# Performance work log

Measured on AMD Instinct MI355X. Metric: run time of the kernel, lower is better.

## Reference

```python
import jax, jax.numpy as jnp
import numpy as np

HEAD_DIM = 32
KSIZE = 3
SCALE = HEAD_DIM ** (-0.5)  # self.scale = head_dim ** -0.5 with head_dim=32


def setup_inputs() -> dict:
    key = jax.random.key(0)
    kq, kk, kv = jax.random.split(key, 3)
    shape = (4, 128, 128, 128)  # (B, d, H, W)
    return {
        "q": jax.random.normal(kq, shape, dtype=jnp.float32),
        "k": jax.random.normal(kk, shape, dtype=jnp.float32),
        "v": jax.random.normal(kv, shape, dtype=jnp.float32),
    }


def _unfold3(x):
    # nn.Unfold(kernel_size=3, dilation=1, padding=1, stride=1):
    # [B, d, H, W] -> [B, d, 9, H, W], kernel positions in row-major (ki, kj)
    B, d, H, W = x.shape
    xp = jnp.pad(x, ((0, 0), (0, 0), (1, 1), (1, 1)))
    return jnp.stack(
        [xp[:, :, i:i + H, j:j + W] for i in range(KSIZE) for j in range(KSIZE)],
        axis=2,
    )


def reference(q, k, v):
    B, d, H, W = q.shape
    h = d // HEAD_DIM  # number of heads
    n = H * W
    # q: [B, h, head_dim, n]
    qh = q.reshape(B, h, HEAD_DIM, n)
    # k patches: [B, h, head_dim, 9, n]
    kp = _unfold3(k).reshape(B, h, HEAD_DIM, KSIZE * KSIZE, n)
    # attn: [B, h, n, 9] = (q . k_neighbor) * scale, softmax over the 9 neighbors
    attn = jnp.einsum('bhcn,bhckn->bhnk', qh, kp) * SCALE
    attn = jax.nn.softmax(attn, axis=-1)
    # v patches: [B, h, head_dim, 9, n]
    vp = _unfold3(v).reshape(B, h, HEAD_DIM, KSIZE * KSIZE, n)
    # out: [B, n, h, head_dim] -> [B, H, W, d] (head-major channel layout, as in torch)
    out = jnp.einsum('bhnk,bhckn->bnhc', attn, vp).reshape(B, H, W, d)
    return jax.nn.relu(out)
```

## Files before the change

kernel.cpp:

```cpp
#include <hip/hip_runtime.h>

#define HW 128
#define PLANE (HW * HW)
#define SCALE 0.17677669529663687f

__global__ __launch_bounds__(256, 2) void natt3x3_kernel(
    const float* __restrict__ q,
    const float* __restrict__ k,
    const float* __restrict__ v,
    float* __restrict__ out) {
  const int tid  = threadIdx.x;
  const int lane = tid & 63;
  const int w    = tid >> 6;
  const int h2   = lane & 1;
  const int s    = lane >> 1;
  const int x0   = s << 2;
  const int bid  = blockIdx.x;
  const int ytile = bid & 31;
  const int head  = (bid >> 5) & 3;
  const int b     = bid >> 7;
  const int y     = (ytile << 2) | w;

  const size_t cbase = (size_t)(b * 128 + head * 32 + h2 * 4) * PLANE;
  const int yx = y * HW + x0;

  int yrow[3];
#pragma unroll
  for (int dy = 0; dy < 3; ++dy) {
    int yy = y + dy - 1; yy = yy < 0 ? 0 : (yy > HW - 1 ? HW - 1 : yy);
    yrow[dy] = yy * HW;
  }

  float l[4][9];
#pragma unroll
  for (int i = 0; i < 4; ++i)
#pragma unroll
    for (int j = 0; j < 9; ++j) l[i][j] = 0.f;

  float4 qv[2][4];
  float4 kv[2][3][4];
  float4 vv[2][3][4];

#define QK_LOAD(B, G) do {                                                   \
    const size_t cb = cbase + (size_t)((G) * 8) * PLANE;                     \
    const float* qg = q + cb + yx;                                           \
    const float* kg = k + cb;                                                \
    _Pragma("unroll")                                                        \
    for (int c = 0; c < 4; ++c) {                                            \
      qv[B][c] = *reinterpret_cast<const float4*>(qg + (size_t)c * PLANE);   \
      _Pragma("unroll")                                                      \
      for (int dy = 0; dy < 3; ++dy)                                         \
        kv[B][dy][c] = *reinterpret_cast<const float4*>(                     \
            kg + (size_t)c * PLANE + yrow[dy] + x0);                         \
    }                                                                        \
  } while (0)

#define QK_COMP(B) do {                                                      \
    _Pragma("unroll")                                                        \
    for (int c = 0; c < 4; ++c) {                                            \
      const float qa[4] = {qv[B][c].x * SCALE, qv[B][c].y * SCALE,           \
                           qv[B][c].z * SCALE, qv[B][c].w * SCALE};          \
      _Pragma("unroll")                                                      \
      for (int dy = 0; dy < 3; ++dy) {                                       \
        float4 kq = kv[B][dy][c];                                            \
        float n0 = __shfl_up(kq.w, 2);                                       \
        float n5 = __shfl_down(kq.x, 2);                                     \
        const float n[6] = {n0, kq.x, kq.y, kq.z, kq.w, n5};                 \
        _Pragma("unroll")                                                    \
        for (int i = 0; i < 4; ++i)                                          \
          _Pragma("unroll")                                                  \
          for (int j = 0; j < 3; ++j)                                        \
            l[i][dy * 3 + j] += qa[i] * n[i + j];                            \
      }                                                                      \
    }                                                                        \
  } while (0)

#define PV_LOAD(B, G) do {                                                   \
    const size_t cb = cbase + (size_t)((G) * 8) * PLANE;                     \
    const float* vg = v + cb;                                                \
    _Pragma("unroll")                                                        \
    for (int c = 0; c < 4; ++c)                                              \
      _Pragma("unroll")                                                      \
      for (int dy = 0; dy < 3; ++dy)                                         \
        vv[B][dy][c] = *reinterpret_cast<const float4*>(                     \
            vg + (size_t)c * PLANE + yrow[dy] + x0);                         \
  } while (0)

#define PV_COMP(B, G) do {                                                   \
    float acc[4][4];                                                         \
    _Pragma("unroll")                                                        \
    for (int i = 0; i < 4; ++i)                                              \
      _Pragma("unroll")                                                      \
      for (int c = 0; c < 4; ++c) acc[i][c] = 0.f;                           \
    _Pragma("unroll")                                                        \
    for (int c = 0; c < 4; ++c)                                              \
      _Pragma("unroll")                                                      \
      for (int dy = 0; dy < 3; ++dy) {                                       \
        float4 vq = vv[B][dy][c];                                            \
        float n0 = __shfl_up(vq.w, 2);                                       \
        float n5 = __shfl_down(vq.x, 2);                                     \
        const float n[6] = {n0, vq.x, vq.y, vq.z, vq.w, n5};                 \
        _Pragma("unroll")                                                    \
        for (int i = 0; i < 4; ++i)                                          \
          _Pragma("unroll")                                                  \
          for (int j = 0; j < 3; ++j)                                        \
            acc[i][c] += l[i][dy * 3 + j] * n[i + j];                        \
      }                                                                      \
    _Pragma("unroll")                                                        \
    for (int i = 0; i < 4; ++i) {                                            \
      float4 o;                                                              \
      o.x = fmaxf(acc[i][0], 0.f);                                           \
      o.y = fmaxf(acc[i][1], 0.f);                                           \
      o.z = fmaxf(acc[i][2], 0.f);                                           \
      o.w = fmaxf(acc[i][3], 0.f);                                           \
      *reinterpret_cast<float4*>(out + obase + (size_t)(x0 + i) * 128 +      \
                                 (G) * 8) = o;                               \
    }                                                                        \
  } while (0)

  QK_LOAD(0, 0);
  QK_LOAD(1, 1);
  QK_COMP(0);
  QK_LOAD(0, 2);
  QK_COMP(1);
  QK_LOAD(1, 3);
  QK_COMP(0);
  QK_COMP(1);

  PV_LOAD(0, 0);

#pragma unroll
  for (int i = 0; i < 4; ++i)
#pragma unroll
    for (int j = 0; j < 9; ++j) l[i][j] += __shfl_xor(l[i][j], 1);

#pragma unroll
  for (int i = 0; i < 4; ++i) {
    const int xp = x0 + i;
    float mk[9];
#pragma unroll
    for (int dy = 0; dy < 3; ++dy)
#pragma unroll
      for (int dx = 0; dx < 3; ++dx) {
        bool ok = ((unsigned)(y + dy - 1) < (unsigned)HW) &&
                  ((unsigned)(xp + dx - 1) < (unsigned)HW);
        mk[dy * 3 + dx] = ok ? 1.f : 0.f;
      }
    float m = -1e30f;
#pragma unroll
    for (int j = 0; j < 9; ++j) {
      float t = l[i][j] * mk[j];
      l[i][j] = t;
      m = fmaxf(m, t);
    }
    float sum = 0.f;
#pragma unroll
    for (int j = 0; j < 9; ++j) {
      float e = __expf(l[i][j] - m);
      l[i][j] = e;
      sum += e;
    }
    float inv = 1.f / sum;
#pragma unroll
    for (int j = 0; j < 9; ++j) l[i][j] *= inv * mk[j];
  }

  const size_t obase = ((size_t)(b * PLANE + y * HW)) * 128 + head * 32 + h2 * 4;

  PV_LOAD(1, 1);
  PV_COMP(0, 0);
  PV_LOAD(0, 2);
  PV_COMP(1, 1);
  PV_LOAD(1, 3);
  PV_COMP(0, 2);
  PV_COMP(1, 3);

#undef QK_LOAD
#undef QK_COMP
#undef PV_LOAD
#undef PV_COMP
}

extern "C" void kernel_launch(void* const* d_in, const int* in_sizes, int n_in,
                              void* d_out, int out_size, void* d_ws, size_t ws_size,
                              hipStream_t stream) {
  const float* q = (const float*)d_in[0];
  const float* k = (const float*)d_in[1];
  const float* v = (const float*)d_in[2];
  float* out = (float*)d_out;
  natt3x3_kernel<<<512, 256, 0, stream>>>(q, k, v, out);
}
```

Before: 33.44 us.

## Deepen load pipeline to three stages with shared K/V register ring and fences

Moves from double buffering to a three-slot register ring shared between K and V tiles, so more global loads are in flight ahead of compute. V loads for the first groups are issued during the QK phase, before the softmax. Compiler memory fences pin the schedule order. This raises register pressure, which under launch_bounds(256,2) could cause spills, and the fences may block useful reordering by the compiler.

Measured after the change: 34.62 us. 1.04x slower.

```diff
diff --git a/kernel.cpp b/kernel.cpp
--- a/kernel.cpp
+++ b/kernel.cpp
@@ -3,6 +3,7 @@
 #define HW 128
 #define PLANE (HW * HW)
 #define SCALE 0.17677669529663687f
+#define FENCE() asm volatile("" ::: "memory")
 
 __global__ __launch_bounds__(256, 2) void natt3x3_kernel(
     const float* __restrict__ q,
@@ -37,32 +38,42 @@
 #pragma unroll
     for (int j = 0; j < 9; ++j) l[i][j] = 0.f;
 
-  float4 qv[2][4];
-  float4 kv[2][3][4];
-  float4 vv[2][3][4];
+  float4 qv4[3][4];
+  float4 rv[3][3][4];
 
-#define QK_LOAD(B, G) do {                                                   \
+#define LQK(B, G) do {                                                       \
     const size_t cb = cbase + (size_t)((G) * 8) * PLANE;                     \
     const float* qg = q + cb + yx;                                           \
     const float* kg = k + cb;                                                \
     _Pragma("unroll")                                                        \
-    for (int c = 0; c < 4; ++c) {                                            \
-      qv[B][c] = *reinterpret_cast<const float4*>(qg + (size_t)c * PLANE);   \
+    for (int c = 0; c < 4; ++c)                                              \
+      qv4[B][c] = *reinterpret_cast<const float4*>(qg + (size_t)c * PLANE);  \
+    _Pragma("unroll")                                                        \
+    for (int c = 0; c < 4; ++c)                                              \
       _Pragma("unroll")                                                      \
       for (int dy = 0; dy < 3; ++dy)                                         \
-        kv[B][dy][c] = *reinterpret_cast<const float4*>(                     \
+        rv[B][dy][c] = *reinterpret_cast<const float4*>(                     \
             kg + (size_t)c * PLANE + yrow[dy] + x0);                         \
-    }                                                                        \
   } while (0)
 
-#define QK_COMP(B) do {                                                      \
+#define LPV(B, G) do {                                                       \
+    const float* vg = v + cbase + (size_t)((G) * 8) * PLANE;                 \
+    _Pragma("unroll")                                                        \
+    for (int c = 0; c < 4; ++c)                                              \
+      _Pragma("unroll")                                                      \
+      for (int dy = 0; dy < 3; ++dy)                                         \
+        rv[B][dy][c] = *reinterpret_cast<const float4*>(                     \
+            vg + (size_t)c * PLANE + yrow[dy] + x0);                         \
+  } while (0)
+
+#define CQK(B) do {                                                          \
     _Pragma("unroll")                                                        \
     for (int c = 0; c < 4; ++c) {                                            \
-      const float qa[4] = {qv[B][c].x * SCALE, qv[B][c].y * SCALE,           \
-                           qv[B][c].z * SCALE, qv[B][c].w * SCALE};          \
+      const float qa[4] = {qv4[B][c].x * SCALE, qv4[B][c].y * SCALE,         \
+                           qv4[B][c].z * SCALE, qv4[B][c].w * SCALE};        \
       _Pragma("unroll")                                                      \
       for (int dy = 0; dy < 3; ++dy) {                                       \
-        float4 kq = kv[B][dy][c];                                            \
+        float4 kq = rv[B][dy][c];                                            \
         float n0 = __shfl_up(kq.w, 2);                                       \
         float n5 = __shfl_down(kq.x, 2);                                     \
         const float n[6] = {n0, kq.x, kq.y, kq.z, kq.w, n5};                 \
@@ -75,18 +86,7 @@
     }                                                                        \
   } while (0)
 
-#define PV_LOAD(B, G) do {                                                   \
-    const size_t cb = cbase + (size_t)((G) * 8) * PLANE;                     \
-    const float* vg = v + cb;                                                \
-    _Pragma("unroll")                                                        \
-    for (int c = 0; c < 4; ++c)                                              \
-      _Pragma("unroll")                                                      \
-      for (int dy = 0; dy < 3; ++dy)                                         \
-        vv[B][dy][c] = *reinterpret_cast<const float4*>(                     \
-            vg + (size_t)c * PLANE + yrow[dy] + x0);                         \
-  } while (0)
-
-#define PV_COMP(B, G) do {                                                   \
+#define CPV(B, G) do {                                                       \
     float acc[4][4];                                                         \
     _Pragma("unroll")                                                        \
     for (int i = 0; i < 4; ++i)                                              \
@@ -96,7 +96,7 @@
     for (int c = 0; c < 4; ++c)                                              \
       _Pragma("unroll")                                                      \
       for (int dy = 0; dy < 3; ++dy) {                                       \
-        float4 vq = vv[B][dy][c];                                            \
+        float4 vq = rv[B][dy][c];                                            \
         float n0 = __shfl_up(vq.w, 2);                                       \
         float n5 = __shfl_down(vq.x, 2);                                     \
         const float n[6] = {n0, vq.x, vq.y, vq.z, vq.w, n5};                 \
@@ -118,16 +118,19 @@
     }                                                                        \
   } while (0)
 
-  QK_LOAD(0, 0);
-  QK_LOAD(1, 1);
-  QK_COMP(0);
-  QK_LOAD(0, 2);
-  QK_COMP(1);
-  QK_LOAD(1, 3);
-  QK_COMP(0);
-  QK_COMP(1);
+  const size_t obase = ((size_t)(b * PLANE + y * HW)) * 128 + head * 32 + h2 * 4;
 
-  PV_LOAD(0, 0);
+  LQK(0, 0); FENCE();
+  LQK(1, 1); FENCE();
+  LQK(2, 2); FENCE();
+  CQK(0);    FENCE();
+  LQK(0, 3); FENCE();
+  CQK(1);    FENCE();
+  LPV(1, 0); FENCE();
+  CQK(2);    FENCE();
+  LPV(2, 1); FENCE();
+  CQK(0);    FENCE();
+  LPV(0, 2); FENCE();
 
 #pragma unroll
   for (int i = 0; i < 4; ++i)
@@ -164,21 +167,18 @@
 #pragma unroll
     for (int j = 0; j < 9; ++j) l[i][j] *= inv * mk[j];
   }
+  FENCE();
 
-  const size_t obase = ((size_t)(b * PLANE + y * HW)) * 128 + head * 32 + h2 * 4;
+  CPV(1, 0); FENCE();
+  LPV(1, 3); FENCE();
+  CPV(2, 1); FENCE();
+  CPV(0, 2); FENCE();
+  CPV(1, 3);
 
-  PV_LOAD(1, 1);
-  PV_COMP(0, 0);
-  PV_LOAD(0, 2);
-  PV_COMP(1, 1);
-  PV_LOAD(1, 3);
-  PV_COMP(0, 2);
-  PV_COMP(1, 3);
-
-#undef QK_LOAD
-#undef QK_COMP
-#undef PV_LOAD
-#undef PV_COMP
+#undef LQK
+#undef LPV
+#undef CQK
+#undef CPV
 }
 
 extern "C" void kernel_launch(void* const* d_in, const int* in_sizes, int n_in,
```
